# Optimization experiments

Hardware: AMD Instinct MI355X
Metric: run time of the kernel (lower is better)

Reference implementation:

```python
import jax, jax.numpy as jnp
import numpy as np

H_DIM, W_DIM, D_MODEL = 128, 128, 1024
N_HEADS, HEAD_DIM = 16, 64


def setup_inputs() -> dict:
    key = jax.random.key(0)
    ks = jax.random.split(key, 8)
    s = D_MODEL ** -0.5
    return {
        "hidden_state": jax.random.normal(ks[0], (H_DIM, W_DIM, D_MODEL), jnp.float32),
        "attn_mask": jnp.zeros((1, 1, W_DIM, W_DIM), jnp.float32),
        "cos": jax.random.uniform(ks[1], (H_DIM, W_DIM, 1, HEAD_DIM), jnp.float32),
        "sin": jax.random.uniform(ks[2], (H_DIM, W_DIM, 1, HEAD_DIM), jnp.float32),
        "Wq": jax.random.normal(ks[3], (D_MODEL, N_HEADS * HEAD_DIM), jnp.float32) * s,
        "Wk": jax.random.normal(ks[4], (D_MODEL, N_HEADS * HEAD_DIM), jnp.float32) * s,
        "Wv": jax.random.normal(ks[5], (D_MODEL, N_HEADS * HEAD_DIM), jnp.float32) * s,
        "Wo": jax.random.normal(ks[6], (2 * D_MODEL, D_MODEL), jnp.float32) * s,
    }


def _rotate_half(x):
    x1, x2 = jnp.split(x, 2, axis=-1)
    return jnp.concatenate((-x2, x1), axis=-1)


def reference(hidden_state, attn_mask, cos, sin, Wq, Wk, Wv, Wo):
    h, w, d = hidden_state.shape
    Dh = cos.shape[-1]
    nH = d // Dh
    # projections (no bias) + RoPE on q/k
    q = (hidden_state @ Wq).reshape(h, w, nH, Dh)
    k = (hidden_state @ Wk).reshape(h, w, nH, Dh)
    v = (hidden_state @ Wv).reshape(h, w, nH, Dh)
    q = q * cos + _rotate_half(q) * sin
    k = k * cos + _rotate_half(k) * sin
    # NOTE: original divides by sqrt(hidden_size), not sqrt(head_dim)
    scale = jnp.sqrt(jnp.asarray(d, hidden_state.dtype))
    # ---- width attention: (h, w, nH, Dh) -> (h, nH, w, Dh) ----
    qx, kx, vx = (t.transpose(0, 2, 1, 3) for t in (q, k, v))
    sx = jnp.einsum('ahqd,ahkd->ahqk', qx, kx) / scale + attn_mask  # (h, nH, w, w)
    ow = jnp.einsum('ahqk,ahkd->ahqd', jax.nn.softmax(sx, axis=-1), vx)
    w_weights = ow.transpose(0, 2, 1, 3)  # (h, w, nH, Dh)
    # ---- height attention: (h, w, nH, Dh) -> (w, nH, h, Dh) ----
    qy, ky, vy = (t.transpose(1, 2, 0, 3) for t in (q, k, v))
    my = jnp.transpose(attn_mask, (2, 1, 0, 3))
    sy = jnp.einsum('ahqd,ahkd->ahqk', qy, ky) / scale + my  # (w, nH, h, h)
    oh = jnp.einsum('ahqk,ahkd->ahqd', jax.nn.softmax(sy, axis=-1), vy)
    h_weights = oh.transpose(2, 0, 1, 3)  # (h, w, nH, Dh)
    cat = jnp.concatenate([w_weights.reshape(h, w, d), h_weights.reshape(h, w, d)], axis=-1)
    return cat @ Wo
```

## Files before the change

### kernel.cpp

```cpp
#include <hip/hip_runtime.h>

typedef unsigned short u16;
typedef unsigned int   u32;
typedef __bf16 bf16;
typedef bf16  bf16x8 __attribute__((ext_vector_type(8)));
typedef float f32x4  __attribute__((ext_vector_type(4)));

__device__ __forceinline__ u16 bf16u(float f) {
    u32 x = __builtin_bit_cast(u32, f);
    x += 0x7fffu + ((x >> 16) & 1u);
    return (u16)(x >> 16);
}

__device__ __forceinline__ void gl_lds16(const void* g, void* l) {
    __builtin_amdgcn_global_load_lds(
        (const __attribute__((address_space(1))) u32*)g,
        (__attribute__((address_space(3))) u32*)l, 16, 0, 0);
}

__global__ __launch_bounds__(256) void cvt_x_kernel(const float4* __restrict__ in,
                                                    ushort4* __restrict__ out, int n4) {
    int i = blockIdx.x * 256 + threadIdx.x;
    if (i >= n4) return;
    float4 f = in[i];
    ushort4 o;
    o.x = bf16u(f.x); o.y = bf16u(f.y); o.z = bf16u(f.z); o.w = bf16u(f.w);
    out[i] = o;
}

__global__ __launch_bounds__(256) void transp_kernel(const float* __restrict__ W,
                                                     u16* __restrict__ WT,
                                                     int rows, int cols) {
    __shared__ float t[32][33];
    int bx = blockIdx.x * 32, by = blockIdx.y * 32;
    int x = threadIdx.x & 31, y = threadIdx.x >> 5;
#pragma unroll
    for (int i = 0; i < 32; i += 8)
        t[y + i][x] = W[(size_t)(by + y + i) * cols + bx + x];
    __syncthreads();
#pragma unroll
    for (int i = 0; i < 32; i += 8)
        WT[(size_t)(bx + y + i) * rows + by + x] = bf16u(t[x][y + i]);
}

#define BK2 32
__global__ __launch_bounds__(512, 2) void gemm8(
    const u16* __restrict__ A, const u16* __restrict__ BT, void* __restrict__ Cout,
    const float* __restrict__ cosp, const float* __restrict__ sinp,
    int M, int N, int K, int mode)
{
    __shared__ u16 Al[4][256 * BK2];
    __shared__ u16 Bl[4][256 * BK2];
    const int tid = threadIdx.x;
    const int wid = tid >> 6, lane = tid & 63;
    const int nx = gridDim.x;
    const int nwg = nx * gridDim.y;
    const int orig = blockIdx.y * nx + blockIdx.x;
    const int vid = (orig & 7) * (nwg >> 3) + (orig >> 3);
    const int m0 = (vid / nx) << 8, n0 = (vid % nx) << 8;
    const int wr = wid >> 2, wc = wid & 3;

    const int c0 = tid, c1 = 512 + tid;
    const int r0 = c0 >> 2, r1 = c1 >> 2;
    const int ch0 = (c0 & 3) ^ ((r0 >> 1) & 3);
    const int ch1 = (c1 & 3) ^ ((r1 >> 1) & 3);
    const u16* aS0 = A + (size_t)(m0 + r0) * K + (ch0 << 3);
    const u16* aS1 = A + (size_t)(m0 + r1) * K + (ch1 << 3);
    const u16* bS0 = BT + (size_t)(n0 + r0) * K + (ch0 << 3);
    const u16* bS1 = BT + (size_t)(n0 + r1) * K + (ch1 << 3);
    const int ldsw = wid << 9;

#define STAGE(tt) do { int _b = (tt) & 3; size_t _ko = (size_t)(tt) * BK2; \
        gl_lds16(aS0 + _ko, &Al[_b][ldsw]);         \
        gl_lds16(aS1 + _ko, &Al[_b][4096 + ldsw]);  \
        gl_lds16(bS0 + _ko, &Bl[_b][ldsw]);         \
        gl_lds16(bS1 + _ko, &Bl[_b][4096 + ldsw]);  } while (0)

    const int nt = K >> 5;
    STAGE(0); STAGE(1); STAGE(2);

    const int ch_rd = (((lane >> 4) ^ ((lane >> 1) & 3)) << 3);
    const int ra = (wr << 7) + (lane & 15);
    const int rb = (wc << 6) + (lane & 15);

    f32x4 acc[8][4] = {};

    for (int t = 0; t < nt; ++t) {
        asm volatile("s_waitcnt lgkmcnt(0)" ::: "memory");
        if (t + 2 < nt)      asm volatile("s_waitcnt vmcnt(8)" ::: "memory");
        else if (t + 1 < nt) asm volatile("s_waitcnt vmcnt(4)" ::: "memory");
        else                 asm volatile("s_waitcnt vmcnt(0)" ::: "memory");
        __builtin_amdgcn_s_barrier();
        if (t + 3 < nt) STAGE(t + 3);

        const u16* Ab = &Al[t & 3][0];
        const u16* Bb = &Bl[t & 3][0];
        bf16x8 af[8], bfr[4];
#pragma unroll
        for (int mi = 0; mi < 8; mi++)
            af[mi] = *(const bf16x8*)&Ab[((ra + (mi << 4)) << 5) + ch_rd];
#pragma unroll
        for (int ni = 0; ni < 4; ni++)
            bfr[ni] = *(const bf16x8*)&Bb[((rb + (ni << 4)) << 5) + ch_rd];

        __builtin_amdgcn_s_setprio(1);
#pragma unroll
        for (int mi = 0; mi < 8; mi++)
#pragma unroll
            for (int ni = 0; ni < 4; ni++)
                acc[mi][ni] = __builtin_amdgcn_mfma_f32_16x16x32_bf16(af[mi], bfr[ni], acc[mi][ni], 0, 0, 0);
        __builtin_amdgcn_s_setprio(0);
    }
#undef STAGE

    const int colbase = n0 + (wc << 6) + (lane & 15);
    if (mode == 2) {
        float* C = (float*)Cout;
#pragma unroll
        for (int mi = 0; mi < 8; mi++)
#pragma unroll
            for (int r = 0; r < 4; r++) {
                int m = m0 + (wr << 7) + (mi << 4) + ((lane >> 4) << 2) + r;
                float* row = C + (size_t)m * N + colbase;
#pragma unroll
                for (int ni = 0; ni < 4; ni++) row[ni << 4] = acc[mi][ni][r];
            }
    } else if (n0 < 2048) {
        u16* C = (u16*)Cout;
#pragma unroll
        for (int mi = 0; mi < 8; mi++)
#pragma unroll
            for (int r = 0; r < 4; r++) {
                int m = m0 + (wr << 7) + (mi << 4) + ((lane >> 4) << 2) + r;
                const float* cb = cosp + ((size_t)m << 6);
                const float* sb = sinp + ((size_t)m << 6);
                u16* row = C + (size_t)m * N + colbase;
#pragma unroll
                for (int ni = 0; ni < 4; ni++) {
                    int d = (ni << 4) + (lane & 15);
                    float c = cb[d], s = sb[d];
                    float v0 = acc[mi][ni][r];
                    float vr = acc[mi][ni ^ 2][r];
                    float o = fmaf(v0, c, (ni < 2 ? -vr : vr) * s);
                    row[ni << 4] = bf16u(o);
                }
            }
    } else {
        u16* C = (u16*)Cout;
#pragma unroll
        for (int mi = 0; mi < 8; mi++)
#pragma unroll
            for (int r = 0; r < 4; r++) {
                int m = m0 + (wr << 7) + (mi << 4) + ((lane >> 4) << 2) + r;
                u16* row = C + (size_t)m * N + colbase;
#pragma unroll
                for (int ni = 0; ni < 4; ni++) row[ni << 4] = bf16u(acc[mi][ni][r]);
            }
    }
}

__global__ __launch_bounds__(256) void axial_attn(
    const u16* __restrict__ qkv, const float* __restrict__ mask,
    u16* __restrict__ cat, int hmode)
{
    __shared__ u16 Kl[128 * 64];
    __shared__ u16 VT[64 * 128];
    __shared__ u16 Pl[128 * 128];
    const int orig = blockIdx.x;
    const int b = (orig & 7) * 256 + (orig >> 3);
    const int a = b >> 4, hd = b & 15;
    const int tid = threadIdx.x, wid = tid >> 6, lane = tid & 63;
    const int tmul = hmode ? 128 : 1;
    const int tadd = hmode ? a : (a << 7);
    const size_t hoff = (size_t)hd << 6;

#pragma unroll
    for (int c = 0; c < 4; c++) {
        int row = (wid << 5) + (c << 3) + (lane >> 3);
        int sc = (lane & 7) ^ (row & 7);
        gl_lds16(qkv + (size_t)(row * tmul + tadd) * 3072 + 1024 + hoff + (sc << 3),
                 &Kl[((wid << 5) + (c << 3)) << 6]);
    }
#pragma unroll
    for (int i = 0; i < 4; i++) {
        int cid = tid + (i << 8);
        int j = cid >> 3;
        int d0 = (cid & 7) << 3;
        uint4 raw = *(const uint4*)(qkv + (size_t)(j * tmul + tadd) * 3072 + 2048 + hoff + d0);
        const u16* e = (const u16*)&raw;
#pragma unroll
        for (int t = 0; t < 8; t++) {
            int d = d0 + t;
            VT[(d << 7) + (((j >> 3) ^ (d & 15)) << 3) + (j & 7)] = e[t];
        }
    }
    bf16x8 aq[2][2];
#pragma unroll
    for (int qt = 0; qt < 2; qt++)
#pragma unroll
        for (int ks = 0; ks < 2; ks++) {
            int row = (wid << 5) + (qt << 4) + (lane & 15);
            aq[qt][ks] = *(const bf16x8*)(qkv + (size_t)(row * tmul + tadd) * 3072 + hoff
                                          + (ks << 5) + ((lane >> 4) << 3));
        }
    __syncthreads();

    f32x4 S[2][8] = {};
#pragma unroll
    for (int kt = 0; kt < 8; kt++) {
        bf16x8 bk[2];
#pragma unroll
        for (int ks = 0; ks < 2; ks++) {
            int row = (kt << 4) + (lane & 15);
            int ch = ((ks << 2) + (lane >> 4)) ^ (row & 7);
            bk[ks] = *(const bf16x8*)&Kl[(row << 6) + (ch << 3)];
        }
#pragma unroll
        for (int qt = 0; qt < 2; qt++) {
            S[qt][kt] = __builtin_amdgcn_mfma_f32_16x16x32_bf16(aq[qt][0], bk[0], S[qt][kt], 0, 0, 0);
            S[qt][kt] = __builtin_amdgcn_mfma_f32_16x16x32_bf16(aq[qt][1], bk[1], S[qt][kt], 0, 0, 0);
        }
    }

    const float scale = 0.03125f;
#pragma unroll
    for (int qt = 0; qt < 2; qt++) {
#pragma unroll
        for (int r = 0; r < 4; r++) {
            int qrow = (wid << 5) + (qt << 4) + ((lane >> 4) << 2) + r;
            const float* mrow = mask + (hmode ? (a << 7) : (qrow << 7));
            float mx = -1e30f;
#pragma unroll
            for (int kt = 0; kt < 8; kt++) {
                float sv = fmaf(S[qt][kt][r], scale, mrow[(kt << 4) + (lane & 15)]);
                S[qt][kt][r] = sv;
                mx = fmaxf(mx, sv);
            }
            mx = fmaxf(mx, __shfl_xor(mx, 1));
            mx = fmaxf(mx, __shfl_xor(mx, 2));
            mx = fmaxf(mx, __shfl_xor(mx, 4));
            mx = fmaxf(mx, __shfl_xor(mx, 8));
            float sum = 0.f;
#pragma unroll
            for (int kt = 0; kt < 8; kt++) {
                float p = __expf(S[qt][kt][r] - mx);
                S[qt][kt][r] = p;
                sum += p;
            }
            sum += __shfl_xor(sum, 1);
            sum += __shfl_xor(sum, 2);
            sum += __shfl_xor(sum, 4);
            sum += __shfl_xor(sum, 8);
            float rinv = 1.0f / sum;
#pragma unroll
            for (int kt = 0; kt < 8; kt++) {
                int kcol = (kt << 4) + (lane & 15);
                int ch = (kcol >> 3) ^ (qrow & 15);
                Pl[(qrow << 7) + (ch << 3) + (kcol & 7)] = bf16u(S[qt][kt][r] * rinv);
            }
        }
    }
    __syncthreads();

    f32x4 O[4][2] = {};
#pragma unroll
    for (int ks = 0; ks < 4; ks++) {
        bf16x8 av[4], bp[2];
#pragma unroll
        for (int dt = 0; dt < 4; dt++) {
            int drow = (dt << 4) + (lane & 15);
            int ch = ((ks << 2) + (lane >> 4)) ^ (drow & 15);
            av[dt] = *(const bf16x8*)&VT[(drow << 7) + (ch << 3)];
        }
#pragma unroll
        for (int qt = 0; qt < 2; qt++) {
            int qrow = (wid << 5) + (qt << 4) + (lane & 15);
            int ch = ((ks << 2) + (lane >> 4)) ^ (qrow & 15);
            bp[qt] = *(const bf16x8*)&Pl[(qrow << 7) + (ch << 3)];
        }
#pragma unroll
        for (int dt = 0; dt < 4; dt++)
#pragma unroll
            for (int qt = 0; qt < 2; qt++)
                O[dt][qt] = __builtin_amdgcn_mfma_f32_16x16x32_bf16(av[dt], bp[qt], O[dt][qt], 0, 0, 0);
    }

    const int cbase = (hmode ? 1024 : 0) + (hd << 6);
#pragma unroll
    for (int dt = 0; dt < 4; dt++)
#pragma unroll
        for (int qt = 0; qt < 2; qt++) {
            int qrow = (wid << 5) + (qt << 4) + (lane & 15);
            int d0 = (dt << 4) + ((lane >> 4) << 2);
            size_t base = ((size_t)(qrow * tmul + tadd) << 11) + cbase + d0;
            ushort4 pk;
            pk.x = bf16u(O[dt][qt][0]);
            pk.y = bf16u(O[dt][qt][1]);
            pk.z = bf16u(O[dt][qt][2]);
            pk.w = bf16u(O[dt][qt][3]);
            *(ushort4*)(cat + base) = pk;
        }
}

extern "C" void kernel_launch(void* const* d_in, const int* in_sizes, int n_in,
                              void* d_out, int out_size, void* d_ws, size_t ws_size,
                              hipStream_t stream)
{
    (void)in_sizes; (void)n_in; (void)out_size; (void)ws_size;
    const float* hidden = (const float*)d_in[0];
    const float* mask   = (const float*)d_in[1];
    const float* cosp   = (const float*)d_in[2];
    const float* sinp   = (const float*)d_in[3];
    const float* Wq     = (const float*)d_in[4];
    const float* Wk     = (const float*)d_in[5];
    const float* Wv     = (const float*)d_in[6];
    const float* Wo     = (const float*)d_in[7];

    char* ws = (char*)d_ws;
    u16* Xb    = (u16*)(ws);
    u16* WqkvT = (u16*)(ws + 33554432);
    u16* cat   = (u16*)(ws);
    u16* WoT   = (u16*)(ws + 67108864);
    u16* qkvb  = (u16*)(ws + 71303168);

    cvt_x_kernel<<<16384, 256, 0, stream>>>((const float4*)hidden, (ushort4*)Xb, 4194304);

    transp_kernel<<<dim3(32, 32), 256, 0, stream>>>(Wq, WqkvT,               1024, 1024);
    transp_kernel<<<dim3(32, 32), 256, 0, stream>>>(Wk, WqkvT + 1024 * 1024, 1024, 1024);
    transp_kernel<<<dim3(32, 32), 256, 0, stream>>>(Wv, WqkvT + 2048 * 1024, 1024, 1024);
    transp_kernel<<<dim3(32, 64), 256, 0, stream>>>(Wo, WoT, 2048, 1024);

    gemm8<<<dim3(12, 64), 512, 0, stream>>>(Xb, WqkvT, qkvb, cosp, sinp, 16384, 3072, 1024, 1);

    axial_attn<<<2048, 256, 0, stream>>>(qkvb, mask, cat, 0);
    axial_attn<<<2048, 256, 0, stream>>>(qkvb, mask, cat, 1);

    gemm8<<<dim3(4, 64), 512, 0, stream>>>(cat, WoT, d_out, nullptr, nullptr, 16384, 1024, 2048, 2);
}
```

Before: 362.0 us.

## Restructure GEMM main loop into BK=64 double-buffered ping-pong with interleaved staging

Replaces the 4-stage BK=32 pipeline in the bf16 GEMM with a 2-buffer BK=64 scheme. Each tile is split into half-tiles, and LDS reads, global-to-LDS loads and MFMA quadrants are interleaved, with barriers between each sub-step. The LDS swizzle changes to an 8-chunk XOR pattern to suit the wider rows. The aim is to overlap memory staging with MFMA work at finer granularity and to halve the number of loop iterations. The cost is many extra barriers and fragile vmcnt accounting that could stall or race.

```diff
diff --git a/kernel.cpp b/kernel.cpp
--- a/kernel.cpp
+++ b/kernel.cpp
@@ -43,14 +43,53 @@
         WT[(size_t)(bx + y + i) * rows + by + x] = bf16u(t[x][y + i]);
 }
 
-#define BK2 32
+__device__ __forceinline__ void rd_a(const u16* base, int lane, int ch0, int ch1,
+                                     int mh, bf16x8* fa) {
+#pragma unroll
+    for (int q = 0; q < 4; q++) {
+        int off = (((mh << 2) + q) << 10) + ((lane & 15) << 6);
+        fa[2 * q]     = *(const bf16x8*)&base[off + ch0];
+        fa[2 * q + 1] = *(const bf16x8*)&base[off + ch1];
+    }
+}
+__device__ __forceinline__ void rd_b(const u16* base, int lane, int ch0, int ch1,
+                                     int rbase, int nh, bf16x8* fb) {
+#pragma unroll
+    for (int q = 0; q < 2; q++) {
+        int off = rbase + (((nh << 1) + q) << 10) + ((lane & 15) << 6);
+        fb[2 * q]     = *(const bf16x8*)&base[off + ch0];
+        fb[2 * q + 1] = *(const bf16x8*)&base[off + ch1];
+    }
+}
+__device__ __forceinline__ void mm16(f32x4 (&acc)[8][4], const bf16x8* fa,
+                                     const bf16x8* fb, int mh, int nh) {
+    __builtin_amdgcn_s_setprio(1);
+#pragma unroll
+    for (int q = 0; q < 4; q++)
+#pragma unroll
+        for (int p = 0; p < 2; p++) {
+            f32x4 c = acc[(mh << 2) + q][(nh << 1) + p];
+            c = __builtin_amdgcn_mfma_f32_16x16x32_bf16(fa[2 * q],     fb[2 * p],     c, 0, 0, 0);
+            c = __builtin_amdgcn_mfma_f32_16x16x32_bf16(fa[2 * q + 1], fb[2 * p + 1], c, 0, 0, 0);
+            acc[(mh << 2) + q][(nh << 1) + p] = c;
+        }
+    __builtin_amdgcn_s_setprio(0);
+}
+
+#define BAR   __builtin_amdgcn_s_barrier()
+#define SB0   __builtin_amdgcn_sched_barrier(0)
+#define LGKM0 asm volatile("s_waitcnt lgkmcnt(0)" ::: "memory")
+#define VM6   asm volatile("s_waitcnt vmcnt(6)" ::: "memory")
+#define VM4   asm volatile("s_waitcnt vmcnt(4)" ::: "memory")
+#define VM0   asm volatile("s_waitcnt vmcnt(0)" ::: "memory")
+
 __global__ __launch_bounds__(512, 2) void gemm8(
     const u16* __restrict__ A, const u16* __restrict__ BT, void* __restrict__ Cout,
     const float* __restrict__ cosp, const float* __restrict__ sinp,
     int M, int N, int K, int mode)
 {
-    __shared__ u16 Al[4][256 * BK2];
-    __shared__ u16 Bl[4][256 * BK2];
+    __shared__ u16 Al[2][2][8192];
+    __shared__ u16 Bl[2][2][8192];
     const int tid = threadIdx.x;
     const int wid = tid >> 6, lane = tid & 63;
     const int nx = gridDim.x;
@@ -59,59 +98,69 @@
     const int vid = (orig & 7) * (nwg >> 3) + (orig >> 3);
     const int m0 = (vid / nx) << 8, n0 = (vid % nx) << 8;
     const int wr = wid >> 2, wc = wid & 3;
-
-    const int c0 = tid, c1 = 512 + tid;
-    const int r0 = c0 >> 2, r1 = c1 >> 2;
-    const int ch0 = (c0 & 3) ^ ((r0 >> 1) & 3);
-    const int ch1 = (c1 & 3) ^ ((r1 >> 1) & 3);
-    const u16* aS0 = A + (size_t)(m0 + r0) * K + (ch0 << 3);
-    const u16* aS1 = A + (size_t)(m0 + r1) * K + (ch1 << 3);
-    const u16* bS0 = BT + (size_t)(n0 + r0) * K + (ch0 << 3);
-    const u16* bS1 = BT + (size_t)(n0 + r1) * K + (ch1 << 3);
-    const int ldsw = wid << 9;
-
-#define STAGE(tt) do { int _b = (tt) & 3; size_t _ko = (size_t)(tt) * BK2; \
-        gl_lds16(aS0 + _ko, &Al[_b][ldsw]);         \
-        gl_lds16(aS1 + _ko, &Al[_b][4096 + ldsw]);  \
-        gl_lds16(bS0 + _ko, &Bl[_b][ldsw]);         \
-        gl_lds16(bS1 + _ko, &Bl[_b][4096 + ldsw]);  } while (0)
-
-    const int nt = K >> 5;
-    STAGE(0); STAGE(1); STAGE(2);
-
-    const int ch_rd = (((lane >> 4) ^ ((lane >> 1) & 3)) << 3);
-    const int ra = (wr << 7) + (lane & 15);
-    const int rb = (wc << 6) + (lane & 15);
+    const int wch = wc >> 1, rbB = (wc & 1) << 12;
+
+    const int sr = tid >> 3;
+    const int sg = (tid & 7) ^ (sr & 7);
+    const u16* Asrc = A + (size_t)(m0 + sr) * K + (sg << 3);
+    const u16* Bsrc = BT + (size_t)(n0 + sr) * K + (sg << 3);
+    const size_t hK   = (size_t)128 * K;
+    const size_t h64K = (size_t)64 * K;
+    const int db = wid << 9;
+    const int nt = K >> 6;
+
+#define STGA(T, h) do { if ((T) < nt) { \
+        const u16* _s = Asrc + (size_t)(h) * hK + ((size_t)(T) << 6); \
+        gl_lds16(_s,        &Al[(T) & 1][h][db]); \
+        gl_lds16(_s + h64K, &Al[(T) & 1][h][4096 + db]); } } while (0)
+#define STGB(T, h) do { if ((T) < nt) { \
+        const u16* _s = Bsrc + (size_t)(h) * hK + ((size_t)(T) << 6); \
+        gl_lds16(_s,        &Bl[(T) & 1][h][db]); \
+        gl_lds16(_s + h64K, &Bl[(T) & 1][h][4096 + db]); } } while (0)
+
+    const int ch0 = (((lane >> 4))     ^ (lane & 7)) << 3;
+    const int ch1 = (((lane >> 4) + 4) ^ (lane & 7)) << 3;
 
     f32x4 acc[8][4] = {};
 
-    for (int t = 0; t < nt; ++t) {
-        asm volatile("s_waitcnt lgkmcnt(0)" ::: "memory");
-        if (t + 2 < nt)      asm volatile("s_waitcnt vmcnt(8)" ::: "memory");
-        else if (t + 1 < nt) asm volatile("s_waitcnt vmcnt(4)" ::: "memory");
-        else                 asm volatile("s_waitcnt vmcnt(0)" ::: "memory");
-        __builtin_amdgcn_s_barrier();
-        if (t + 3 < nt) STAGE(t + 3);
-
-        const u16* Ab = &Al[t & 3][0];
-        const u16* Bb = &Bl[t & 3][0];
-        bf16x8 af[8], bfr[4];
-#pragma unroll
-        for (int mi = 0; mi < 8; mi++)
-            af[mi] = *(const bf16x8*)&Ab[((ra + (mi << 4)) << 5) + ch_rd];
-#pragma unroll
-        for (int ni = 0; ni < 4; ni++)
-            bfr[ni] = *(const bf16x8*)&Bb[((rb + (ni << 4)) << 5) + ch_rd];
-
-        __builtin_amdgcn_s_setprio(1);
-#pragma unroll
-        for (int mi = 0; mi < 8; mi++)
-#pragma unroll
-            for (int ni = 0; ni < 4; ni++)
-                acc[mi][ni] = __builtin_amdgcn_mfma_f32_16x16x32_bf16(af[mi], bfr[ni], acc[mi][ni], 0, 0, 0);
-        __builtin_amdgcn_s_setprio(0);
-    }
-#undef STAGE
+    STGA(0, 0); STGA(0, 1); STGB(0, 0); STGB(0, 1);
+    STGB(1, 0); STGA(1, 0);
+    VM4;
+    BAR; SB0;
+
+    const int nt2 = nt >> 1;
+    for (int i = 0; i < nt2; ++i) {
+        const int Tb = 2 * i + 1, Tc = 2 * i + 2, Td = 2 * i + 3;
+        bf16x8 fa[8], fb[4], fc[4];
+        rd_a(&Al[0][wr][0], lane, ch0, ch1, 0, fa);
+        rd_b(&Bl[0][wch][0], lane, ch0, ch1, rbB, 0, fb);
+        STGA(Tb, 1); STGB(Tb, 1);
+        BAR; LGKM0; mm16(acc, fa, fb, 0, 0); BAR;
+        rd_b(&Bl[0][wch][0], lane, ch0, ch1, rbB, 1, fc);
+        BAR; LGKM0; mm16(acc, fa, fc, 0, 1); BAR;
+        rd_a(&Al[0][wr][0], lane, ch0, ch1, 1, fa);
+        STGB(Tc, 0); STGB(Tc, 1);
+        BAR; LGKM0; mm16(acc, fa, fc, 1, 1); BAR;
+        STGA(Tc, 0);
+        BAR; LGKM0; mm16(acc, fa, fb, 1, 0);
+        if (i + 1 < nt2) { VM6; } else { VM0; }
+        BAR; SB0;
+        rd_a(&Al[1][wr][0], lane, ch0, ch1, 0, fa);
+        rd_b(&Bl[1][wch][0], lane, ch0, ch1, rbB, 0, fb);
+        STGA(Tc, 1);
+        BAR; LGKM0; mm16(acc, fa, fb, 0, 0); BAR;
+        rd_b(&Bl[1][wch][0], lane, ch0, ch1, rbB, 1, fc);
+        BAR; LGKM0; mm16(acc, fa, fc, 0, 1); BAR;
+        rd_a(&Al[1][wr][0], lane, ch0, ch1, 1, fa);
+        STGB(Td, 0);
+        BAR; LGKM0; mm16(acc, fa, fc, 1, 1); BAR;
+        STGA(Td, 0);
+        BAR; LGKM0; mm16(acc, fa, fb, 1, 0);
+        VM4;
+        BAR; SB0;
+    }
+#undef STGA
+#undef STGB
 
     const int colbase = n0 + (wc << 6) + (lane & 15);
     if (mode == 2) {
```

New measurement: 327.9 us. 1.1x faster.

## Restructure GEMM main loop into ping-pong phases overlapping LDS reads with MFMA

Applied to the files above, without the earlier changes.

Rewrites the bf16 GEMM inner loop so each K-tile is split into two half-phases. LDS fragment reads for the next half, and the global-to-LDS stages for A and B, are interleaved between barriers with the MFMA work of the current half, using double-buffered register fragments. A and B tiles are merged into one LDS buffer per stage. This aims to hide LDS read latency and spread out global loads, at the cost of four barriers per tile and a loop unrolled by four that assumes the K-tile count is a multiple of four.

```diff
diff --git a/kernel.cpp b/kernel.cpp
--- a/kernel.cpp
+++ b/kernel.cpp
@@ -43,14 +43,42 @@
         WT[(size_t)(bx + y + i) * rows + by + x] = bf16u(t[x][y + i]);
 }
 
-#define BK2 32
+__device__ __forceinline__ void rdA4(const u16* b, int ra, int phys, int mh,
+                                     bf16x8 (&f)[4]) {
+#pragma unroll
+    for (int q = 0; q < 4; q++)
+        f[q] = *(const bf16x8*)&b[ra + (((mh << 2) + q) << 9) + phys];
+}
+__device__ __forceinline__ void rdB4(const u16* b, int rb, int phys,
+                                     bf16x8 (&f)[4]) {
+#pragma unroll
+    for (int q = 0; q < 4; q++)
+        f[q] = *(const bf16x8*)&b[rb + (q << 9) + phys];
+}
+__device__ __forceinline__ void mm16f(f32x4 (&acc)[8][4], int mh,
+                                      const bf16x8 (&fa)[4], const bf16x8 (&fb)[4]) {
+    __builtin_amdgcn_s_setprio(1);
+#pragma unroll
+    for (int m = 0; m < 4; m++)
+#pragma unroll
+        for (int n = 0; n < 4; n++)
+            acc[(mh << 2) + m][n] = __builtin_amdgcn_mfma_f32_16x16x32_bf16(
+                fa[m], fb[n], acc[(mh << 2) + m][n], 0, 0, 0);
+    __builtin_amdgcn_s_setprio(0);
+}
+
+#define BAR   __builtin_amdgcn_s_barrier()
+#define VM8   asm volatile("s_waitcnt vmcnt(8)" ::: "memory")
+#define VM6   asm volatile("s_waitcnt vmcnt(6)" ::: "memory")
+#define VM4   asm volatile("s_waitcnt vmcnt(4)" ::: "memory")
+#define VM0   asm volatile("s_waitcnt vmcnt(0)" ::: "memory")
+
 __global__ __launch_bounds__(512, 2) void gemm8(
     const u16* __restrict__ A, const u16* __restrict__ BT, void* __restrict__ Cout,
     const float* __restrict__ cosp, const float* __restrict__ sinp,
     int M, int N, int K, int mode)
 {
-    __shared__ u16 Al[4][256 * BK2];
-    __shared__ u16 Bl[4][256 * BK2];
+    __shared__ u16 Ld[4][16384];
     const int tid = threadIdx.x;
     const int wid = tid >> 6, lane = tid & 63;
     const int nx = gridDim.x;
@@ -60,58 +88,65 @@
     const int m0 = (vid / nx) << 8, n0 = (vid % nx) << 8;
     const int wr = wid >> 2, wc = wid & 3;
 
-    const int c0 = tid, c1 = 512 + tid;
-    const int r0 = c0 >> 2, r1 = c1 >> 2;
-    const int ch0 = (c0 & 3) ^ ((r0 >> 1) & 3);
-    const int ch1 = (c1 & 3) ^ ((r1 >> 1) & 3);
-    const u16* aS0 = A + (size_t)(m0 + r0) * K + (ch0 << 3);
-    const u16* aS1 = A + (size_t)(m0 + r1) * K + (ch1 << 3);
-    const u16* bS0 = BT + (size_t)(n0 + r0) * K + (ch0 << 3);
-    const u16* bS1 = BT + (size_t)(n0 + r1) * K + (ch1 << 3);
-    const int ldsw = wid << 9;
-
-#define STAGE(tt) do { int _b = (tt) & 3; size_t _ko = (size_t)(tt) * BK2; \
-        gl_lds16(aS0 + _ko, &Al[_b][ldsw]);         \
-        gl_lds16(aS1 + _ko, &Al[_b][4096 + ldsw]);  \
-        gl_lds16(bS0 + _ko, &Bl[_b][ldsw]);         \
-        gl_lds16(bS1 + _ko, &Bl[_b][4096 + ldsw]);  } while (0)
-
+    const int r1 = tid >> 2;
+    const int l1 = (tid & 3) ^ ((r1 >> 1) & 3);
+    const u16* Asrc = A + (size_t)(m0 + r1) * K + (l1 << 3);
+    const u16* Bsrc = BT + (size_t)(n0 + r1) * K + (l1 << 3);
+    const size_t h128K = (size_t)128 * K;
+    const int wdb = wid << 9;
     const int nt = K >> 5;
-    STAGE(0); STAGE(1); STAGE(2);
-
-    const int ch_rd = (((lane >> 4) ^ ((lane >> 1) & 3)) << 3);
-    const int ra = (wr << 7) + (lane & 15);
-    const int rb = (wc << 6) + (lane & 15);
+
+#define STA(T, DB) do { if ((T) < nt) { const u16* _s = Asrc + ((size_t)(T) << 5); \
+        gl_lds16(_s,         &Ld[DB][wdb]); \
+        gl_lds16(_s + h128K, &Ld[DB][4096 + wdb]); } } while (0)
+#define STB(T, DB) do { if ((T) < nt) { const u16* _s = Bsrc + ((size_t)(T) << 5); \
+        gl_lds16(_s,         &Ld[DB][8192 + wdb]); \
+        gl_lds16(_s + h128K, &Ld[DB][12288 + wdb]); } } while (0)
+#define VMPUB(t) do { if ((t) + 3 < nt) { VM6; } \
+                      else if ((t) + 2 < nt) { VM4; } else { VM0; } } while (0)
+
+    const int phys = ((lane >> 4) ^ ((lane >> 1) & 3)) << 3;
+    const int ra = ((wr << 7) + (lane & 15)) << 5;
+    const int rb = ((((wc << 6) + (lane & 15)) << 5)) + 8192;
 
     f32x4 acc[8][4] = {};
-
-    for (int t = 0; t < nt; ++t) {
-        asm volatile("s_waitcnt lgkmcnt(0)" ::: "memory");
-        if (t + 2 < nt)      asm volatile("s_waitcnt vmcnt(8)" ::: "memory");
-        else if (t + 1 < nt) asm volatile("s_waitcnt vmcnt(4)" ::: "memory");
-        else                 asm volatile("s_waitcnt vmcnt(0)" ::: "memory");
-        __builtin_amdgcn_s_barrier();
-        if (t + 3 < nt) STAGE(t + 3);
-
-        const u16* Ab = &Al[t & 3][0];
-        const u16* Bb = &Bl[t & 3][0];
-        bf16x8 af[8], bfr[4];
-#pragma unroll
-        for (int mi = 0; mi < 8; mi++)
-            af[mi] = *(const bf16x8*)&Ab[((ra + (mi << 4)) << 5) + ch_rd];
-#pragma unroll
-        for (int ni = 0; ni < 4; ni++)
-            bfr[ni] = *(const bf16x8*)&Bb[((rb + (ni << 4)) << 5) + ch_rd];
-
-        __builtin_amdgcn_s_setprio(1);
-#pragma unroll
-        for (int mi = 0; mi < 8; mi++)
-#pragma unroll
-            for (int ni = 0; ni < 4; ni++)
-                acc[mi][ni] = __builtin_amdgcn_mfma_f32_16x16x32_bf16(af[mi], bfr[ni], acc[mi][ni], 0, 0, 0);
-        __builtin_amdgcn_s_setprio(0);
-    }
-#undef STAGE
+    bf16x8 faA[4], faB[4], fb0[4], fb1[4];
+
+    STA(0, 0); STB(0, 0); STA(1, 1); STB(1, 1); STA(2, 2); STB(2, 2);
+    VM8;
+    BAR;
+    rdA4(&Ld[0][0], ra, phys, 0, faA);
+    rdB4(&Ld[0][0], rb, phys, fb0);
+
+#define PH_PAIR(t, D, D2, D3, E, F) do { \
+     \
+    rdA4(&Ld[D][0], ra, phys, 1, faB); \
+    STA((t) + 3, D3); \
+    BAR; \
+    mm16f(acc, 0, faA, fb##E); \
+    VMPUB(t); \
+    BAR; \
+     \
+    if ((t) + 1 < nt) { \
+        rdA4(&Ld[D2][0], ra, phys, 0, faA); \
+        rdB4(&Ld[D2][0], rb, phys, fb##F); \
+    } \
+    STB((t) + 3, D3); \
+    BAR; \
+    mm16f(acc, 1, faB, fb##E); \
+    BAR; \
+} while (0)
+
+    for (int t = 0; t < nt; t += 4) {
+        PH_PAIR(t,     0, 1, 3, 0, 1);
+        PH_PAIR(t + 1, 1, 2, 0, 1, 0);
+        PH_PAIR(t + 2, 2, 3, 1, 0, 1);
+        PH_PAIR(t + 3, 3, 0, 2, 1, 0);
+    }
+#undef PH_PAIR
+#undef STA
+#undef STB
+#undef VMPUB
 
     const int colbase = n0 + (wc << 6) + (lane & 15);
     if (mode == 2) {
```

After: 467.6 us. 1.29x slower.

## Restructure GEMM into 3-stage LDS pipeline and merge small kernel launches

Applied to the files above, without the earlier changes.

The GEMM main loop now uses three LDS buffers instead of four. Fragments are read from LDS first, then the next prefetch is issued, and barriers bracket the MFMA block. This lowers LDS use, which may help occupancy, and puts the global-to-LDS loads after the fragment reads, at the cost of two barriers per iteration. Separately, the four weight-transpose launches are fused into one 3D-grid kernel, and the width and height attention launches are fused into a single 4096-block launch, cutting launch overhead and tail idle time.

```diff
diff --git a/kernel.cpp b/kernel.cpp
--- a/kernel.cpp
+++ b/kernel.cpp
@@ -28,9 +28,21 @@
     out[i] = o;
 }
 
-__global__ __launch_bounds__(256) void transp_kernel(const float* __restrict__ W,
-                                                     u16* __restrict__ WT,
-                                                     int rows, int cols) {
+__global__ __launch_bounds__(256) void transp_all(
+    const float* __restrict__ Wq, const float* __restrict__ Wk,
+    const float* __restrict__ Wv, const float* __restrict__ Wo,
+    u16* __restrict__ WqkvT, u16* __restrict__ WoT)
+{
+    const int z = blockIdx.z;
+    const float* W; u16* WT; int rows, cols;
+    if (z < 3) {
+        if (blockIdx.y >= 32) return;
+        W = (z == 0) ? Wq : (z == 1) ? Wk : Wv;
+        WT = WqkvT + (size_t)z * 1024 * 1024;
+        rows = 1024; cols = 1024;
+    } else {
+        W = Wo; WT = WoT; rows = 2048; cols = 1024;
+    }
     __shared__ float t[32][33];
     int bx = blockIdx.x * 32, by = blockIdx.y * 32;
     int x = threadIdx.x & 31, y = threadIdx.x >> 5;
@@ -43,14 +55,17 @@
         WT[(size_t)(bx + y + i) * rows + by + x] = bf16u(t[x][y + i]);
 }
 
-#define BK2 32
+#define BAR   __builtin_amdgcn_s_barrier()
+#define SB0   __builtin_amdgcn_sched_barrier(0)
+#define VM4   asm volatile("s_waitcnt vmcnt(4)" ::: "memory")
+#define VM0   asm volatile("s_waitcnt vmcnt(0)" ::: "memory")
+
 __global__ __launch_bounds__(512, 2) void gemm8(
     const u16* __restrict__ A, const u16* __restrict__ BT, void* __restrict__ Cout,
     const float* __restrict__ cosp, const float* __restrict__ sinp,
     int M, int N, int K, int mode)
 {
-    __shared__ u16 Al[4][256 * BK2];
-    __shared__ u16 Bl[4][256 * BK2];
+    __shared__ u16 Ld[3][16384];
     const int tid = threadIdx.x;
     const int wid = tid >> 6, lane = tid & 63;
     const int nx = gridDim.x;
@@ -60,56 +75,55 @@
     const int m0 = (vid / nx) << 8, n0 = (vid % nx) << 8;
     const int wr = wid >> 2, wc = wid & 3;
 
-    const int c0 = tid, c1 = 512 + tid;
-    const int r0 = c0 >> 2, r1 = c1 >> 2;
-    const int ch0 = (c0 & 3) ^ ((r0 >> 1) & 3);
-    const int ch1 = (c1 & 3) ^ ((r1 >> 1) & 3);
-    const u16* aS0 = A + (size_t)(m0 + r0) * K + (ch0 << 3);
-    const u16* aS1 = A + (size_t)(m0 + r1) * K + (ch1 << 3);
-    const u16* bS0 = BT + (size_t)(n0 + r0) * K + (ch0 << 3);
-    const u16* bS1 = BT + (size_t)(n0 + r1) * K + (ch1 << 3);
-    const int ldsw = wid << 9;
-
-#define STAGE(tt) do { int _b = (tt) & 3; size_t _ko = (size_t)(tt) * BK2; \
-        gl_lds16(aS0 + _ko, &Al[_b][ldsw]);         \
-        gl_lds16(aS1 + _ko, &Al[_b][4096 + ldsw]);  \
-        gl_lds16(bS0 + _ko, &Bl[_b][ldsw]);         \
-        gl_lds16(bS1 + _ko, &Bl[_b][4096 + ldsw]);  } while (0)
-
+    const int srow = tid >> 2;
+    const int sl = (tid & 3) ^ ((srow >> 1) & 3);
+    const u16* aS0 = A + (size_t)(m0 + srow) * K + (sl << 3);
+    const u16* aS1 = aS0 + (size_t)128 * K;
+    const u16* bS0 = BT + (size_t)(n0 + srow) * K + (sl << 3);
+    const u16* bS1 = bS0 + (size_t)128 * K;
+    const int wdb = wid << 9;
     const int nt = K >> 5;
-    STAGE(0); STAGE(1); STAGE(2);
-
-    const int ch_rd = (((lane >> 4) ^ ((lane >> 1) & 3)) << 3);
-    const int ra = (wr << 7) + (lane & 15);
-    const int rb = (wc << 6) + (lane & 15);
+
+#define STAGE(T, B_) do { if ((T) < nt) { size_t _ko = (size_t)(T) << 5; \
+        gl_lds16(aS0 + _ko, &Ld[B_][wdb]); \
+        gl_lds16(aS1 + _ko, &Ld[B_][4096 + wdb]); \
+        gl_lds16(bS0 + _ko, &Ld[B_][8192 + wdb]); \
+        gl_lds16(bS1 + _ko, &Ld[B_][12288 + wdb]); } } while (0)
+
+    const int phys = ((lane >> 4) ^ ((lane >> 1) & 3)) << 3;
+    const int raw = ((wr << 7) + (lane & 15)) << 5;
+    const int rbw = (((wc << 6) + (lane & 15)) << 5) + 8192;
 
     f32x4 acc[8][4] = {};
 
+    STAGE(0, 0); STAGE(1, 1);
+    VM4;
+    BAR; SB0;
+
+    int b = 0, bs = 2;
     for (int t = 0; t < nt; ++t) {
-        asm volatile("s_waitcnt lgkmcnt(0)" ::: "memory");
-        if (t + 2 < nt)      asm volatile("s_waitcnt vmcnt(8)" ::: "memory");
-        else if (t + 1 < nt) asm volatile("s_waitcnt vmcnt(4)" ::: "memory");
-        else                 asm volatile("s_waitcnt vmcnt(0)" ::: "memory");
-        __builtin_amdgcn_s_barrier();
-        if (t + 3 < nt) STAGE(t + 3);
-
-        const u16* Ab = &Al[t & 3][0];
-        const u16* Bb = &Bl[t & 3][0];
-        bf16x8 af[8], bfr[4];
-#pragma unroll
-        for (int mi = 0; mi < 8; mi++)
-            af[mi] = *(const bf16x8*)&Ab[((ra + (mi << 4)) << 5) + ch_rd];
+        const u16* Lb = &Ld[b][0];
+        bf16x8 fa[8], fb[4];
+#pragma unroll
+        for (int mi = 0; mi < 8; mi++)
+            fa[mi] = *(const bf16x8*)&Lb[raw + (mi << 9) + phys];
 #pragma unroll
         for (int ni = 0; ni < 4; ni++)
-            bfr[ni] = *(const bf16x8*)&Bb[((rb + (ni << 4)) << 5) + ch_rd];
-
+            fb[ni] = *(const bf16x8*)&Lb[rbw + (ni << 9) + phys];
+        STAGE(t + 2, bs);
+        BAR;
         __builtin_amdgcn_s_setprio(1);
 #pragma unroll
         for (int mi = 0; mi < 8; mi++)
 #pragma unroll
             for (int ni = 0; ni < 4; ni++)
-                acc[mi][ni] = __builtin_amdgcn_mfma_f32_16x16x32_bf16(af[mi], bfr[ni], acc[mi][ni], 0, 0, 0);
+                acc[mi][ni] = __builtin_amdgcn_mfma_f32_16x16x32_bf16(
+                    fa[mi], fb[ni], acc[mi][ni], 0, 0, 0);
         __builtin_amdgcn_s_setprio(0);
+        if (t + 2 < nt) { VM4; } else { VM0; }
+        BAR; SB0;
+        b = (b == 2) ? 0 : b + 1;
+        bs = (bs == 2) ? 0 : bs + 1;
     }
 #undef STAGE
 
@@ -161,13 +175,14 @@
 
 __global__ __launch_bounds__(256) void axial_attn(
     const u16* __restrict__ qkv, const float* __restrict__ mask,
-    u16* __restrict__ cat, int hmode)
+    u16* __restrict__ cat)
 {
     __shared__ u16 Kl[128 * 64];
     __shared__ u16 VT[64 * 128];
     __shared__ u16 Pl[128 * 128];
-    const int orig = blockIdx.x;
-    const int b = (orig & 7) * 256 + (orig >> 3);
+    const int hmode = blockIdx.x >> 11;
+    const int o2 = blockIdx.x & 2047;
+    const int b = (o2 & 7) * 256 + (o2 >> 3);
     const int a = b >> 4, hd = b & 15;
     const int tid = threadIdx.x, wid = tid >> 6, lane = tid & 63;
     const int tmul = hmode ? 128 : 1;
@@ -324,16 +339,11 @@
     u16* qkvb  = (u16*)(ws + 71303168);
 
     cvt_x_kernel<<<16384, 256, 0, stream>>>((const float4*)hidden, (ushort4*)Xb, 4194304);
-
-    transp_kernel<<<dim3(32, 32), 256, 0, stream>>>(Wq, WqkvT,               1024, 1024);
-    transp_kernel<<<dim3(32, 32), 256, 0, stream>>>(Wk, WqkvT + 1024 * 1024, 1024, 1024);
-    transp_kernel<<<dim3(32, 32), 256, 0, stream>>>(Wv, WqkvT + 2048 * 1024, 1024, 1024);
-    transp_kernel<<<dim3(32, 64), 256, 0, stream>>>(Wo, WoT, 2048, 1024);
+    transp_all<<<dim3(32, 64, 4), 256, 0, stream>>>(Wq, Wk, Wv, Wo, WqkvT, WoT);
 
     gemm8<<<dim3(12, 64), 512, 0, stream>>>(Xb, WqkvT, qkvb, cosp, sinp, 16384, 3072, 1024, 1);
 
-    axial_attn<<<2048, 256, 0, stream>>>(qkvb, mask, cat, 0);
-    axial_attn<<<2048, 256, 0, stream>>>(qkvb, mask, cat, 1);
+    axial_attn<<<4096, 256, 0, stream>>>(qkvb, mask, cat);
 
     gemm8<<<dim3(4, 64), 512, 0, stream>>>(cat, WoT, d_out, nullptr, nullptr, 16384, 1024, 2048, 2);
 }
```

New measurement: 316.9 us. 1.14x faster.
